# Kernel optimization log

Hardware: AMD Instinct MI355X
Metric: run time of the kernel (lower is better)

The kernel has to match this reference:

```python
import jax, jax.numpy as jnp
import numpy as np

# ---- dims (see shape_source) ----
N_NODES = 100_000
N_EDGES = 600_000
N_GRAPHS = 512
N_NODE_FEAT = 90   # atom-type vocabulary
H = 128            # n_hidden_feat
E_FEAT = 256       # n_edge_net_feat
G_FEAT = 128       # n_graph_feat
N_CONV = 3         # n_conv * n_edge_labels, conv_labels = [0,0,0]
SCALE = 0.05


def setup_inputs() -> dict:
    key = jax.random.key(0)
    ks = jax.random.split(key, 16)
    nodes = jax.random.randint(ks[0], (N_NODES,), 0, N_NODE_FEAT)
    edge_sources = jax.random.randint(ks[1], (N_EDGES,), 0, N_NODES)
    edge_targets = jax.random.randint(ks[2], (N_EDGES,), 0, N_NODES)
    graph_indices = jnp.sort(jax.random.randint(ks[3], (N_NODES,), 0, N_GRAPHS))
    node_counts = jnp.maximum(jnp.bincount(graph_indices, length=N_GRAPHS), 1).astype(jnp.float32)

    def rn(k, shape):
        return jax.random.normal(k, shape, jnp.float32) * SCALE

    return {
        "nodes": nodes,
        "edge_sources": edge_sources,
        "edge_targets": edge_targets,
        "graph_indices": graph_indices,
        "node_counts": node_counts,
        # learned parameters
        "embed": rn(ks[4], (N_NODE_FEAT, H)),           # NodeEmbedding table
        "Wg": rn(ks[5], (N_CONV, H, H)),                # gate linear per conv (bias=False)
        "We1": rn(ks[6], (N_CONV, H, E_FEAT)),          # EdgeNetwork layer 1 per conv
        "We2": rn(ks[7], (N_CONV, E_FEAT, H)),          # EdgeNetwork layer 2 per conv
        "Wp": rn(ks[8], (H, H)),                        # LinearPooling
        "Wfc1": rn(ks[9], (H, G_FEAT)), "bfc1": jnp.zeros((G_FEAT,), jnp.float32),
        "Wfc2": rn(ks[10], (G_FEAT, G_FEAT)), "bfc2": jnp.zeros((G_FEAT,), jnp.float32),
        "Wr": rn(ks[11], (G_FEAT, 1)), "br": jnp.zeros((1,), jnp.float32),
    }


def reference(nodes, edge_sources, edge_targets, graph_indices, node_counts,
              embed, Wg, We1, We2, Wp, Wfc1, bfc1, Wfc2, bfc2, Wr, br):
    sp = jax.nn.softplus
    # NodeEmbedding: atom-type lookup -> [N, H]
    x = embed[nodes]
    # Gated graph convolutions: gather -> edge MLP + gate -> scatter-add -> residual
    for i in range(N_CONV):
        z = x[edge_sources]                               # [E, H] gather
        e = sp(z @ We1[i]) @ We2[i]                       # EdgeNetwork (2 layers, no shortcut)
        m = jax.nn.sigmoid(z @ Wg[i]) * sp(e)             # gate * edge_activation(message)
        agg = jax.ops.segment_sum(m, edge_targets, num_segments=N_NODES)  # scatter-add
        x = x + sp(agg)                                   # node_activation + residual
    # LinearPooling (last conv only): per-graph mean of linear(x)
    y = jax.ops.segment_sum(x @ Wp, graph_indices, num_segments=N_GRAPHS) / node_counts[:, None]
    # GraphPooling with n_steps=1: activation only (no batch norm)
    g = sp(y)
    # FullConnection stack (n_fc=2)
    g = sp(g @ Wfc1 + bfc1)
    g = sp(g @ Wfc2 + bfc2)
    return g @ Wr + br
```

## Files before the change

kernel.cpp:

```cpp
#include <hip/hip_runtime.h>
#include <hip/hip_bf16.h>

typedef unsigned short u16;
typedef __attribute__((ext_vector_type(8))) short short8;
typedef __attribute__((ext_vector_type(4))) float f32x4;
typedef __attribute__((ext_vector_type(16))) float f32x16;
typedef __attribute__((ext_vector_type(2))) __bf16 bf16x2;

#define NNODES 100000
#define NEDGES 600000
#define NGRAPHS 512
#define HF 128
#define EF 256
#define XS_LD 136
#define US_LD 264
#define GB 32

__device__ __forceinline__ float bfu(u16 u){ return __uint_as_float(((unsigned)u) << 16); }
__device__ __forceinline__ u16 f2bf(float f){
    unsigned u = __float_as_uint(f);
    unsigned r = (u + 0x7fff + ((u >> 16) & 1)) >> 16;
    return (u16)r;
}
__device__ __forceinline__ unsigned pack2(float a, float b){
    bf16x2 v = { (__bf16)a, (__bf16)b };
    return __builtin_bit_cast(unsigned, v);
}

#if __has_builtin(__builtin_amdgcn_rcpf)
#define RCP1(x) __builtin_amdgcn_rcpf(x)
#else
#define RCP1(x) (1.f / (x))
#endif

__device__ __forceinline__ float sp_f(float x){
    return __logf(1.f + __expf(x));
}
__device__ __forceinline__ float sig_f(float x){
    return RCP1(1.f + __expf(-x));
}
__device__ __forceinline__ float lf(const void* p, long i, bool f32){
    return f32 ? ((const float*)p)[i] : bfu(((const u16*)p)[i]);
}

__device__ __forceinline__ int swz(int row, int ef, int LD){
    int c8 = ef >> 2;
    int s = ((row >> 2) & 3) << 1;
    return row * LD + ((c8 ^ s) << 2) + (ef & 3);
}

__device__ __forceinline__ bool is_f32(const void* probe){
    const u16* p = (const u16*)probe;
    int lane = threadIdx.x & 63;
    int c = 0;
#pragma unroll
    for (int i = 0; i < 4; i++) c += (fabsf(bfu(p[lane * 4 + i])) > 1.0f) ? 1 : 0;
#pragma unroll
    for (int off = 32; off; off >>= 1) c += __shfl_xor(c, off, 64);
    return c > 8;
}

__global__ __launch_bounds__(256) void prep_kernel(const void* __restrict__ wg,
                                                   const void* __restrict__ we1,
                                                   const void* __restrict__ we2,
                                                   const void* __restrict__ wp,
                                                   const void* __restrict__ wfc1,
                                                   const void* __restrict__ wfc2,
                                                   u16* __restrict__ pwg,
                                                   u16* __restrict__ pwe1,
                                                   u16* __restrict__ pwe2,
                                                   u16* __restrict__ pwp,
                                                   u16* __restrict__ pf1,
                                                   u16* __restrict__ pf2,
                                                   const void* __restrict__ emb,
                                                   const int* __restrict__ tgt,
                                                   int* __restrict__ counts){
    int b = blockIdx.x, t = threadIdx.x;
    if (b < 960) {
        bool f32 = is_f32(emb);
        int i = b * 256 + t;
        int c = i / 81920, r = i % 81920;
        const void* src; u16* dst; int N, KN, l;
        if (r < 16384)      { src = wg;  dst = pwg;  N = HF; KN = 16384; l = r; }
        else if (r < 49152) { src = we1; dst = pwe1; N = EF; KN = 32768; l = r - 16384; }
        else                { src = we2; dst = pwe2; N = HF; KN = 32768; l = r - 49152; }
        int j = l & 7, lane = (l >> 3) & 63, rest = l >> 9;
        int NT = N >> 5;
        int nt = rest % NT, ks = rest / NT;
        int k = ks * 16 + (lane >> 5) * 8 + j;
        int n = nt * 32 + (lane & 31);
        long base = (long)c * KN;
        dst[base + l] = f2bf(lf(src, base + (long)k * N + n, f32));
    } else if (b < 1152) {
        bool f32 = is_f32(emb);
        int i = (b - 960) * 256 + t;
        int c = i / 16384, l = i % 16384;
        const void* src = (c == 0) ? wp : (c == 1) ? wfc1 : wfc2;
        u16* dst = (c == 0) ? pwp : (c == 1) ? pf1 : pf2;
        int j = l & 7, lane = (l >> 3) & 63, rest = l >> 9;
        int nt = rest & 7, kt = rest >> 3;
        int k = kt * 32 + (lane >> 4) * 8 + j;
        int n = nt * 16 + (lane & 15);
        dst[l] = f2bf(lf(src, (long)k * HF + n, f32));
    } else {
        int e = (b - 1152) * 256 + t;
        if (e < NEDGES) atomicAdd(&counts[tgt[e]], 1);
    }
}

__global__ __launch_bounds__(256) void scan1_kernel(const int* __restrict__ counts,
                                                    int* __restrict__ row_ptr,
                                                    int* __restrict__ bsums){
    __shared__ int s[256];
    int t = threadIdx.x;
    int i = blockIdx.x * 256 + t;
    int v = (i < NNODES) ? counts[i] : 0;
    s[t] = v; __syncthreads();
    for (int off = 1; off < 256; off <<= 1) {
        int a = (t >= off) ? s[t - off] : 0;
        __syncthreads();
        s[t] += a;
        __syncthreads();
    }
    if (i < NNODES) row_ptr[i] = s[t] - v;
    if (t == 255) bsums[blockIdx.x] = s[255];
}

__global__ __launch_bounds__(512) void scan2_kernel(const int* __restrict__ bsums,
                                                    int* __restrict__ boffs, int nb){
    __shared__ int s[512];
    int t = threadIdx.x;
    int v = (t < nb) ? bsums[t] : 0;
    s[t] = v; __syncthreads();
    for (int off = 1; off < 512; off <<= 1) {
        int a = (t >= off) ? s[t - off] : 0;
        __syncthreads();
        s[t] += a;
        __syncthreads();
    }
    if (t < nb) boffs[t] = s[t] - v;
}

__global__ __launch_bounds__(256) void scan3_kernel(int* __restrict__ row_ptr,
                                                    const int* __restrict__ boffs,
                                                    int* __restrict__ cursor){
    int i = blockIdx.x * 256 + threadIdx.x;
    if (i < NNODES) {
        int r = row_ptr[i] + boffs[blockIdx.x];
        row_ptr[i] = r;
        cursor[i]  = r;
    }
}

__global__ __launch_bounds__(256) void fill_kernel(const int* __restrict__ src,
                                                   const int* __restrict__ tgt,
                                                   int* __restrict__ cursor,
                                                   int* __restrict__ es){
    int e = blockIdx.x * 256 + threadIdx.x;
    if (e < NEDGES) {
        int pos = atomicAdd(&cursor[tgt[e]], 1);
        es[pos] = src[e];
    }
}

__device__ __forceinline__ void conv_phases(u16* xs, u16* us,
                                            const u16* __restrict__ pwg,
                                            const u16* __restrict__ pwe1,
                                            const u16* __restrict__ pwe2,
                                            u16* __restrict__ M, long row0){
    const int t = threadIdx.x;
    const int w = t >> 6, lane = t & 63;
    const int half = lane >> 5, nn = lane & 31;

#pragma unroll
    for (int eft = 0; eft < 2; eft++) {
        int et = w * 2 + eft;
        short8 A[8];
#pragma unroll
        for (int ks = 0; ks < 8; ks++)
            A[ks] = *(const short8*)(pwe1 + (((ks * 8 + et) * 64 + lane) << 3));
#pragma unroll
        for (int nt2 = 0; nt2 < 2; nt2++) {
            f32x16 acc = {};
#pragma unroll
            for (int ks = 0; ks < 8; ks++) {
                short8 B = *(const short8*)(&xs[swz(nt2 * 32 + nn, ks * 16 + half * 8, XS_LD)]);
                acc = __builtin_amdgcn_mfma_f32_32x32x16_bf16(A[ks], B, acc, 0, 0, 0);
            }
#pragma unroll
            for (int q = 0; q < 4; q++) {
                int ef0 = et * 32 + half * 4 + q * 8;
                uint2 d;
                d.x = pack2(sp_f(acc[q*4+0]), sp_f(acc[q*4+1]));
                d.y = pack2(sp_f(acc[q*4+2]), sp_f(acc[q*4+3]));
                *(uint2*)(&us[swz(nt2 * 32 + nn, ef0, US_LD)]) = d;
            }
        }
    }
    __syncthreads();

    {
        f32x16 aT[2] = {{}, {}};
        f32x16 aG[2] = {{}, {}};
#pragma unroll
        for (int ks = 0; ks < 16; ks++) {
            short8 A = *(const short8*)(pwe2 + (((ks * 4 + w) * 64 + lane) << 3));
#pragma unroll
            for (int nt2 = 0; nt2 < 2; nt2++) {
                short8 B = *(const short8*)(&us[swz(nt2 * 32 + nn, ks * 16 + half * 8, US_LD)]);
                aT[nt2] = __builtin_amdgcn_mfma_f32_32x32x16_bf16(A, B, aT[nt2], 0, 0, 0);
            }
        }
#pragma unroll
        for (int ks = 0; ks < 8; ks++) {
            short8 A = *(const short8*)(pwg + (((ks * 4 + w) * 64 + lane) << 3));
#pragma unroll
            for (int nt2 = 0; nt2 < 2; nt2++) {
                short8 B = *(const short8*)(&xs[swz(nt2 * 32 + nn, ks * 16 + half * 8, XS_LD)]);
                aG[nt2] = __builtin_amdgcn_mfma_f32_32x32x16_bf16(A, B, aG[nt2], 0, 0, 0);
            }
        }
#pragma unroll
        for (int nt2 = 0; nt2 < 2; nt2++) {
            long node = row0 + nt2 * 32 + nn;
            if (node < NNODES) {
#pragma unroll
                for (int q = 0; q < 4; q++) {
                    int h0 = w * 32 + half * 4 + q * 8;
                    uint2 d;
                    d.x = pack2(sig_f(aG[nt2][q*4+0]) * sp_f(aT[nt2][q*4+0]),
                                sig_f(aG[nt2][q*4+1]) * sp_f(aT[nt2][q*4+1]));
                    d.y = pack2(sig_f(aG[nt2][q*4+2]) * sp_f(aT[nt2][q*4+2]),
                                sig_f(aG[nt2][q*4+3]) * sp_f(aT[nt2][q*4+3]));
                    *(uint2*)(M + node * HF + h0) = d;
                }
            }
        }
    }
}

__global__ __launch_bounds__(256) void conv0_mfma(const int* __restrict__ nodes,
                                                  const void* __restrict__ emb,
                                                  u16* __restrict__ x,
                                                  const u16* __restrict__ pwg,
                                                  const u16* __restrict__ pwe1,
                                                  const u16* __restrict__ pwe2,
                                                  u16* __restrict__ M){
    __shared__ u16 xs[64 * XS_LD];
    __shared__ u16 us[64 * US_LD];
    const int t = threadIdx.x;
    const long row0 = (long)blockIdx.x * 64;
    const bool f32 = is_f32(emb);

    for (int i = t; i < 4096; i += 256) {
        int r = i >> 6, c = i & 63;
        long node = row0 + r;
        unsigned d = 0u;
        if (node < NNODES) {
            int v = nodes[node];
            if (f32) {
                const float* row = (const float*)emb + (long)v * HF + c * 2;
                d = pack2(row[0], row[1]);
            } else {
                d = ((const unsigned*)emb)[(long)v * 64 + c];
            }
            ((unsigned*)x)[node * 64 + c] = d;
        }
        *(unsigned*)(&xs[swz(r, c * 2, XS_LD)]) = d;
    }
    __syncthreads();
    conv_phases(xs, us, pwg, pwe1, pwe2, M, row0);
}

__global__ __launch_bounds__(256) void conv_mfma(const u16* __restrict__ x,
                                                 const u16* __restrict__ pwg,
                                                 const u16* __restrict__ pwe1,
                                                 const u16* __restrict__ pwe2,
                                                 u16* __restrict__ M){
    __shared__ u16 xs[64 * XS_LD];
    __shared__ u16 us[64 * US_LD];
    const int t = threadIdx.x;
    const long row0 = (long)blockIdx.x * 64;

    for (int i = t; i < 1024; i += 256) {
        int r = i >> 4, q = i & 15;
        long node = row0 + r;
        uint4 v = make_uint4(0u, 0u, 0u, 0u);
        if (node < NNODES) v = *(const uint4*)(x + node * HF + q * 8);
        *(uint4*)(&xs[swz(r, q * 8, XS_LD)]) = v;
    }
    __syncthreads();
    conv_phases(xs, us, pwg, pwe1, pwe2, M, row0);
}

__global__ __launch_bounds__(256) void agg_kernel(const u16* __restrict__ M,
                                                  const int* __restrict__ row_ptr,
                                                  const int* __restrict__ counts,
                                                  const int* __restrict__ es,
                                                  u16* __restrict__ x){
    int wid = blockIdx.x * 4 + (threadIdx.x >> 6);
    int lane = threadIdx.x & 63;
    long v = (long)wid * 4 + (lane >> 4);
    int l = lane & 15;
    if (v >= NNODES) return;
    int start = row_ptr[v], cnt = counts[v];
    float a0=0.f,a1=0.f,a2=0.f,a3=0.f,a4=0.f,a5=0.f,a6=0.f,a7=0.f;
    float b0=0.f,b1=0.f,b2=0.f,b3=0.f,b4=0.f,b5=0.f,b6=0.f,b7=0.f;
    const uint4* Mu = (const uint4*)M;
    int e = 0;
    for (; e + 1 < cnt; e += 2) {
        int s0 = es[start + e], s1 = es[start + e + 1];
        uint4 u0 = Mu[(long)s0 * 16 + l];
        uint4 u1 = Mu[(long)s1 * 16 + l];
        a0 += bfu((u16)u0.x); a1 += bfu((u16)(u0.x >> 16));
        a2 += bfu((u16)u0.y); a3 += bfu((u16)(u0.y >> 16));
        a4 += bfu((u16)u0.z); a5 += bfu((u16)(u0.z >> 16));
        a6 += bfu((u16)u0.w); a7 += bfu((u16)(u0.w >> 16));
        b0 += bfu((u16)u1.x); b1 += bfu((u16)(u1.x >> 16));
        b2 += bfu((u16)u1.y); b3 += bfu((u16)(u1.y >> 16));
        b4 += bfu((u16)u1.z); b5 += bfu((u16)(u1.z >> 16));
        b6 += bfu((u16)u1.w); b7 += bfu((u16)(u1.w >> 16));
    }
    if (e < cnt) {
        int s0 = es[start + e];
        uint4 u0 = Mu[(long)s0 * 16 + l];
        a0 += bfu((u16)u0.x); a1 += bfu((u16)(u0.x >> 16));
        a2 += bfu((u16)u0.y); a3 += bfu((u16)(u0.y >> 16));
        a4 += bfu((u16)u0.z); a5 += bfu((u16)(u0.z >> 16));
        a6 += bfu((u16)u0.w); a7 += bfu((u16)(u0.w >> 16));
    }
    a0 += b0; a1 += b1; a2 += b2; a3 += b3;
    a4 += b4; a5 += b5; a6 += b6; a7 += b7;
    uint4* xu = (uint4*)x;
    uint4 xv = xu[v * 16 + l];
    xv.x = pack2(bfu((u16)xv.x) + sp_f(a0), bfu((u16)(xv.x >> 16)) + sp_f(a1));
    xv.y = pack2(bfu((u16)xv.y) + sp_f(a2), bfu((u16)(xv.y >> 16)) + sp_f(a3));
    xv.z = pack2(bfu((u16)xv.z) + sp_f(a4), bfu((u16)(xv.z >> 16)) + sp_f(a5));
    xv.w = pack2(bfu((u16)xv.w) + sp_f(a6), bfu((u16)(xv.w >> 16)) + sp_f(a7));
    xu[v * 16 + l] = xv;
}

__global__ __launch_bounds__(256) void pool_kernel(const u16* __restrict__ x,
                                                   const int* __restrict__ gidx,
                                                   float* __restrict__ xsum){
    int wave = blockIdx.x * 4 + (threadIdx.x >> 6);
    int lane = threadIdx.x & 63;
    long base = (long)wave * 64;
    if (base >= NNODES) return;
    long end = base + 64; if (end > NNODES) end = NNODES;
    const unsigned* xu = (const unsigned*)x;
    int gcur = gidx[base];
    float a0 = 0.f, a1 = 0.f;
    for (long v = base; v < end; v++) {
        int g = gidx[v];
        if (g != gcur) {
            atomicAdd(&xsum[gcur * HF + lane * 2 + 0], a0);
            atomicAdd(&xsum[gcur * HF + lane * 2 + 1], a1);
            a0 = a1 = 0.f; gcur = g;
        }
        unsigned u = xu[v * 64 + lane];
        a0 += bfu((u16)u);
        a1 += bfu((u16)(u >> 16));
    }
    atomicAdd(&xsum[gcur * HF + lane * 2 + 0], a0);
    atomicAdd(&xsum[gcur * HF + lane * 2 + 1], a1);
}

__global__ __launch_bounds__(256) void head_mfma(const float* __restrict__ xsum,
                                                 const void* __restrict__ ncnt,
                                                 const u16* __restrict__ pwp,
                                                 const u16* __restrict__ pf1,
                                                 const u16* __restrict__ pf2,
                                                 const void* __restrict__ bfc1,
                                                 const void* __restrict__ bfc2,
                                                 const void* __restrict__ Wr,
                                                 const void* __restrict__ br,
                                                 void* __restrict__ out,
                                                 const void* __restrict__ probe){
    __shared__ u16 hibuf[2][GB][136];
    __shared__ u16 lobuf[2][GB][136];
    const int t = threadIdx.x;
    const int w = t >> 6, lane = t & 63;
    const int quad = lane >> 4, nr = lane & 15;
    const bool f32 = is_f32(probe);
    const int g0 = blockIdx.x * GB;

    for (int i = t; i < GB * 64; i += 256) {
        int g = i >> 6, c = (i & 63) * 2;
        float f0 = xsum[(g0 + g) * HF + c], f1 = xsum[(g0 + g) * HF + c + 1];
        u16 h0 = f2bf(f0), h1 = f2bf(f1);
        *(unsigned*)&hibuf[0][g][c] = (unsigned)h0 | ((unsigned)h1 << 16);
        *(unsigned*)&lobuf[0][g][c] = pack2(f0 - bfu(h0), f1 - bfu(h1));
    }
    __syncthreads();

    float rc[2];
#pragma unroll
    for (int nt = 0; nt < 2; nt++) rc[nt] = RCP1(lf(ncnt, g0 + nt * 16 + nr, f32));

    int cur = 0;
    for (int layer = 0; layer < 3; layer++) {
        const u16* pw = (layer == 0) ? pwp : (layer == 1) ? pf1 : pf2;
        const void* bias = (layer == 1) ? bfc1 : bfc2;
        int nxt = cur ^ 1;
#pragma unroll
        for (int c = 0; c < 2; c++) {
            int et = w * 2 + c;
            short8 A[4];
#pragma unroll
            for (int kt = 0; kt < 4; kt++)
                A[kt] = *(const short8*)(pw + (((kt * 8 + et) * 64 + lane) << 3));
#pragma unroll
            for (int nt = 0; nt < 2; nt++) {
                f32x4 acc = {0.f, 0.f, 0.f, 0.f};
#pragma unroll
                for (int kt = 0; kt < 4; kt++) {
                    short8 bh = *(const short8*)(&hibuf[cur][nt * 16 + nr][kt * 32 + quad * 8]);
                    short8 bl = *(const short8*)(&lobuf[cur][nt * 16 + nr][kt * 32 + quad * 8]);
                    acc = __builtin_amdgcn_mfma_f32_16x16x32_bf16(A[kt], bh, acc, 0, 0, 0);
                    acc = __builtin_amdgcn_mfma_f32_16x16x32_bf16(A[kt], bl, acc, 0, 0, 0);
                }
                int feat0 = et * 16 + quad * 4;
                float f[4];
#pragma unroll
                for (int r = 0; r < 4; r++) {
                    float a = (layer == 0) ? acc[r] * rc[nt]
                                           : acc[r] + lf(bias, feat0 + r, f32);
                    f[r] = sp_f(a);
                }
                u16 h[4]; float lo[4];
#pragma unroll
                for (int r = 0; r < 4; r++) { h[r] = f2bf(f[r]); lo[r] = f[r] - bfu(h[r]); }
                uint2 dh, dl;
                dh.x = (unsigned)h[0] | ((unsigned)h[1] << 16);
                dh.y = (unsigned)h[2] | ((unsigned)h[3] << 16);
                dl.x = pack2(lo[0], lo[1]);
                dl.y = pack2(lo[2], lo[3]);
                *(uint2*)&hibuf[nxt][nt * 16 + nr][feat0] = dh;
                *(uint2*)&lobuf[nxt][nt * 16 + nr][feat0] = dl;
            }
        }
        __syncthreads();
        cur = nxt;
    }

    int g = t >> 3, sub = t & 7;
    float p = 0.f;
    for (int k = sub * 16; k < sub * 16 + 16; k++) {
        float v = bfu(hibuf[cur][g][k]) + bfu(lobuf[cur][g][k]);
        p += v * lf(Wr, k, f32);
    }
    p += __shfl_down(p, 4, 64);
    p += __shfl_down(p, 2, 64);
    p += __shfl_down(p, 1, 64);
    if (sub == 0) {
        float res = p + lf(br, 0, f32);
        if (f32) ((float*)out)[g0 + g] = res;
        else     ((u16*)out)[g0 + g]  = f2bf(res);
    }
}

extern "C" void kernel_launch(void* const* d_in, const int* in_sizes, int n_in,
                              void* d_out, int out_size, void* d_ws, size_t ws_size,
                              hipStream_t stream) {
    const int* nodes = (const int*)d_in[0];
    const int* esrc  = (const int*)d_in[1];
    const int* etgt  = (const int*)d_in[2];
    const int* gidx  = (const int*)d_in[3];

    size_t off = 0;
    char* w = (char*)d_ws;
    auto take = [&](size_t bytes) -> void* {
        void* p = w + off;
        off = (off + bytes + 255) & ~(size_t)255;
        return p;
    };

    u16* pwg     = (u16*)take((size_t)3 * HF * HF * 2);
    u16* pwe1    = (u16*)take((size_t)3 * HF * EF * 2);
    u16* pwe2    = (u16*)take((size_t)3 * EF * HF * 2);
    u16* pwp     = (u16*)take((size_t)HF * HF * 2);
    u16* pf1     = (u16*)take((size_t)HF * HF * 2);
    u16* pf2     = (u16*)take((size_t)HF * HF * 2);
    int* counts  = (int*)take((size_t)NNODES * 4);
    int* row_ptr = (int*)take((size_t)NNODES * 4);
    int* cursor  = (int*)take((size_t)NNODES * 4);
    int* es      = (int*)take((size_t)NEDGES * 4);
    int* bsums   = (int*)take(2048);
    int* boffs   = (int*)take(2048);
    float* xsum  = (float*)take((size_t)NGRAPHS * HF * 4);
    u16* x       = (u16*)take((size_t)NNODES * HF * 2);
    u16* M       = (u16*)take((size_t)NNODES * HF * 2);

    hipMemsetAsync(counts, 0, (size_t)NNODES * 4, stream);
    hipMemsetAsync(xsum, 0, (size_t)NGRAPHS * HF * 4, stream);

    prep_kernel<<<3496, 256, 0, stream>>>(d_in[6], d_in[7], d_in[8],
                                          d_in[9], d_in[10], d_in[12],
                                          pwg, pwe1, pwe2, pwp, pf1, pf2,
                                          d_in[5], etgt, counts);

    const int NB_SCAN = (NNODES + 255) / 256;
    const int NB_EDGE = (NEDGES + 255) / 256;
    scan1_kernel<<<NB_SCAN, 256, 0, stream>>>(counts, row_ptr, bsums);
    scan2_kernel<<<1, 512, 0, stream>>>(bsums, boffs, NB_SCAN);
    scan3_kernel<<<NB_SCAN, 256, 0, stream>>>(row_ptr, boffs, cursor);
    fill_kernel<<<NB_EDGE, 256, 0, stream>>>(esrc, etgt, cursor, es);

    const int NBC = (NNODES + 63) / 64;
    const int NBA = (NNODES + 15) / 16;
    conv0_mfma<<<NBC, 256, 0, stream>>>(nodes, d_in[5], x, pwg, pwe1, pwe2, M);
    agg_kernel<<<NBA, 256, 0, stream>>>(M, row_ptr, counts, es, x);
    conv_mfma<<<NBC, 256, 0, stream>>>(x,
        pwg + (size_t)1 * HF * HF, pwe1 + (size_t)1 * HF * EF, pwe2 + (size_t)1 * EF * HF, M);
    agg_kernel<<<NBA, 256, 0, stream>>>(M, row_ptr, counts, es, x);
    conv_mfma<<<NBC, 256, 0, stream>>>(x,
        pwg + (size_t)2 * HF * HF, pwe1 + (size_t)2 * HF * EF, pwe2 + (size_t)2 * EF * HF, M);
    agg_kernel<<<NBA, 256, 0, stream>>>(M, row_ptr, counts, es, x);

    pool_kernel<<<(NNODES + 255) / 256, 256, 0, stream>>>(x, gidx, xsum);
    head_mfma<<<NGRAPHS / GB, 256, 0, stream>>>(xsum, d_in[4], pwp, pf1, pf2,
                                                d_in[11], d_in[13], d_in[14], d_in[15],
                                                d_out, d_in[5]);
}
```

Measured before the change: 424.8 us.

## Switch LDS tiles to chunk-major padded layout and unroll aggregation by four

Replaces the XOR-swizzled row-major shared-memory tiles with a chunk-major layout (8-element chunks, each chunk holding all 64 rows, padded stride 520) for both the node tile and the edge-hidden tile. The goal is conflict-free contiguous 16-byte B-operand reads for the MFMA and simpler index math. The embedding load in conv0 is widened to 16-byte vector loads. The gather-sum in the aggregation kernel is unrolled to four edges per iteration to keep more loads in flight, at the cost of more registers.

```diff
diff --git a/kernel.cpp b/kernel.cpp
--- a/kernel.cpp
+++ b/kernel.cpp
@@ -12,9 +12,10 @@
 #define NGRAPHS 512
 #define HF 128
 #define EF 256
-#define XS_LD 136
-#define US_LD 264
 #define GB 32
+
+#define PLD 520
+__device__ __forceinline__ int cidx(int chunk, int row){ return chunk * PLD + row * 8; }
 
 __device__ __forceinline__ float bfu(u16 u){ return __uint_as_float(((unsigned)u) << 16); }
 __device__ __forceinline__ u16 f2bf(float f){
@@ -41,12 +42,6 @@
 }
 __device__ __forceinline__ float lf(const void* p, long i, bool f32){
     return f32 ? ((const float*)p)[i] : bfu(((const u16*)p)[i]);
-}
-
-__device__ __forceinline__ int swz(int row, int ef, int LD){
-    int c8 = ef >> 2;
-    int s = ((row >> 2) & 3) << 1;
-    return row * LD + ((c8 ^ s) << 2) + (ef & 3);
 }
 
 __device__ __forceinline__ bool is_f32(const void* probe){
@@ -184,16 +179,15 @@
             f32x16 acc = {};
 #pragma unroll
             for (int ks = 0; ks < 8; ks++) {
-                short8 B = *(const short8*)(&xs[swz(nt2 * 32 + nn, ks * 16 + half * 8, XS_LD)]);
+                short8 B = *(const short8*)(&xs[cidx(ks * 2 + half, nt2 * 32 + nn)]);
                 acc = __builtin_amdgcn_mfma_f32_32x32x16_bf16(A[ks], B, acc, 0, 0, 0);
             }
 #pragma unroll
             for (int q = 0; q < 4; q++) {
-                int ef0 = et * 32 + half * 4 + q * 8;
                 uint2 d;
                 d.x = pack2(sp_f(acc[q*4+0]), sp_f(acc[q*4+1]));
                 d.y = pack2(sp_f(acc[q*4+2]), sp_f(acc[q*4+3]));
-                *(uint2*)(&us[swz(nt2 * 32 + nn, ef0, US_LD)]) = d;
+                *(uint2*)(&us[cidx(et * 4 + q, nt2 * 32 + nn) + half * 4]) = d;
             }
         }
     }
@@ -207,7 +201,7 @@
             short8 A = *(const short8*)(pwe2 + (((ks * 4 + w) * 64 + lane) << 3));
 #pragma unroll
             for (int nt2 = 0; nt2 < 2; nt2++) {
-                short8 B = *(const short8*)(&us[swz(nt2 * 32 + nn, ks * 16 + half * 8, US_LD)]);
+                short8 B = *(const short8*)(&us[cidx(ks * 2 + half, nt2 * 32 + nn)]);
                 aT[nt2] = __builtin_amdgcn_mfma_f32_32x32x16_bf16(A, B, aT[nt2], 0, 0, 0);
             }
         }
@@ -216,7 +210,7 @@
             short8 A = *(const short8*)(pwg + (((ks * 4 + w) * 64 + lane) << 3));
 #pragma unroll
             for (int nt2 = 0; nt2 < 2; nt2++) {
-                short8 B = *(const short8*)(&xs[swz(nt2 * 32 + nn, ks * 16 + half * 8, XS_LD)]);
+                short8 B = *(const short8*)(&xs[cidx(ks * 2 + half, nt2 * 32 + nn)]);
                 aG[nt2] = __builtin_amdgcn_mfma_f32_32x32x16_bf16(A, B, aG[nt2], 0, 0, 0);
             }
         }
@@ -246,27 +240,29 @@
                                                   const u16* __restrict__ pwe1,
                                                   const u16* __restrict__ pwe2,
                                                   u16* __restrict__ M){
-    __shared__ u16 xs[64 * XS_LD];
-    __shared__ u16 us[64 * US_LD];
+    __shared__ u16 xs[16 * PLD];
+    __shared__ u16 us[32 * PLD];
     const int t = threadIdx.x;
     const long row0 = (long)blockIdx.x * 64;
     const bool f32 = is_f32(emb);
 
-    for (int i = t; i < 4096; i += 256) {
-        int r = i >> 6, c = i & 63;
+    for (int i = t; i < 1024; i += 256) {
+        int r = i >> 4, q = i & 15;
         long node = row0 + r;
-        unsigned d = 0u;
+        uint4 d = make_uint4(0u, 0u, 0u, 0u);
         if (node < NNODES) {
             int v = nodes[node];
             if (f32) {
-                const float* row = (const float*)emb + (long)v * HF + c * 2;
-                d = pack2(row[0], row[1]);
+                float4 f0 = ((const float4*)emb)[(long)v * 32 + q * 2];
+                float4 f1 = ((const float4*)emb)[(long)v * 32 + q * 2 + 1];
+                d.x = pack2(f0.x, f0.y); d.y = pack2(f0.z, f0.w);
+                d.z = pack2(f1.x, f1.y); d.w = pack2(f1.z, f1.w);
             } else {
-                d = ((const unsigned*)emb)[(long)v * 64 + c];
-            }
-            ((unsigned*)x)[node * 64 + c] = d;
-        }
-        *(unsigned*)(&xs[swz(r, c * 2, XS_LD)]) = d;
+                d = ((const uint4*)emb)[(long)v * 16 + q];
+            }
+            ((uint4*)x)[node * 16 + q] = d;
+        }
+        *(uint4*)(&xs[cidx(q, r)]) = d;
     }
     __syncthreads();
     conv_phases(xs, us, pwg, pwe1, pwe2, M, row0);
@@ -277,8 +273,8 @@
                                                  const u16* __restrict__ pwe1,
                                                  const u16* __restrict__ pwe2,
                                                  u16* __restrict__ M){
-    __shared__ u16 xs[64 * XS_LD];
-    __shared__ u16 us[64 * US_LD];
+    __shared__ u16 xs[16 * PLD];
+    __shared__ u16 us[32 * PLD];
     const int t = threadIdx.x;
     const long row0 = (long)blockIdx.x * 64;
 
@@ -286,8 +282,8 @@
         int r = i >> 4, q = i & 15;
         long node = row0 + r;
         uint4 v = make_uint4(0u, 0u, 0u, 0u);
-        if (node < NNODES) v = *(const uint4*)(x + node * HF + q * 8);
-        *(uint4*)(&xs[swz(r, q * 8, XS_LD)]) = v;
+        if (node < NNODES) v = ((const uint4*)x)[node * 16 + q];
+        *(uint4*)(&xs[cidx(q, r)]) = v;
     }
     __syncthreads();
     conv_phases(xs, us, pwg, pwe1, pwe2, M, row0);
@@ -308,10 +304,13 @@
     float b0=0.f,b1=0.f,b2=0.f,b3=0.f,b4=0.f,b5=0.f,b6=0.f,b7=0.f;
     const uint4* Mu = (const uint4*)M;
     int e = 0;
-    for (; e + 1 < cnt; e += 2) {
-        int s0 = es[start + e], s1 = es[start + e + 1];
+    for (; e + 3 < cnt; e += 4) {
+        int s0 = es[start + e],     s1 = es[start + e + 1];
+        int s2 = es[start + e + 2], s3 = es[start + e + 3];
         uint4 u0 = Mu[(long)s0 * 16 + l];
         uint4 u1 = Mu[(long)s1 * 16 + l];
+        uint4 u2 = Mu[(long)s2 * 16 + l];
+        uint4 u3 = Mu[(long)s3 * 16 + l];
         a0 += bfu((u16)u0.x); a1 += bfu((u16)(u0.x >> 16));
         a2 += bfu((u16)u0.y); a3 += bfu((u16)(u0.y >> 16));
         a4 += bfu((u16)u0.z); a5 += bfu((u16)(u0.z >> 16));
@@ -320,8 +319,16 @@
         b2 += bfu((u16)u1.y); b3 += bfu((u16)(u1.y >> 16));
         b4 += bfu((u16)u1.z); b5 += bfu((u16)(u1.z >> 16));
         b6 += bfu((u16)u1.w); b7 += bfu((u16)(u1.w >> 16));
-    }
-    if (e < cnt) {
+        a0 += bfu((u16)u2.x); a1 += bfu((u16)(u2.x >> 16));
+        a2 += bfu((u16)u2.y); a3 += bfu((u16)(u2.y >> 16));
+        a4 += bfu((u16)u2.z); a5 += bfu((u16)(u2.z >> 16));
+        a6 += bfu((u16)u2.w); a7 += bfu((u16)(u2.w >> 16));
+        b0 += bfu((u16)u3.x); b1 += bfu((u16)(u3.x >> 16));
+        b2 += bfu((u16)u3.y); b3 += bfu((u16)(u3.y >> 16));
+        b4 += bfu((u16)u3.z); b5 += bfu((u16)(u3.z >> 16));
+        b6 += bfu((u16)u3.w); b7 += bfu((u16)(u3.w >> 16));
+    }
+    for (; e < cnt; e++) {
         int s0 = es[start + e];
         uint4 u0 = Mu[(long)s0 * 16 + l];
         a0 += bfu((u16)u0.x); a1 += bfu((u16)(u0.x >> 16));
```

Result: faster. 413.7 us (-2.6%).
